# Performance work log

Measured on AMD Instinct MI355X. Metric: run time of the kernel, lower is better.

The kernel has to match this reference:

```python
import jax, jax.numpy as jnp
import numpy as np

B, S, H = 4, 8192, 576
I = 512   # moe_intermediate_size
E = 8     # num routed experts
TOP_K = 2

def setup_inputs() -> dict:
    key = jax.random.key(0)
    ks = jax.random.split(key, 8)
    sc = lambda fan_in: 1.0 / np.sqrt(fan_in)
    return {
        'x': jax.random.normal(ks[0], (B, S, H), dtype=jnp.float32),
        'shared_gate_w': jax.random.normal(ks[1], (H, I), dtype=jnp.float32) * sc(H),
        'shared_up_w':   jax.random.normal(ks[2], (H, I), dtype=jnp.float32) * sc(H),
        'shared_down_w': jax.random.normal(ks[3], (I, H), dtype=jnp.float32) * sc(I),
        'routed_gate_w': jax.random.normal(ks[4], (E, H, I), dtype=jnp.float32) * sc(H),
        'routed_up_w':   jax.random.normal(ks[5], (E, H, I), dtype=jnp.float32) * sc(H),
        'routed_down_w': jax.random.normal(ks[6], (E, I, H), dtype=jnp.float32) * sc(I),
        'router_w':      jax.random.normal(ks[7], (H, E), dtype=jnp.float32) * sc(H),
        'router_bias':   jnp.zeros((E,), dtype=jnp.float32),
    }

def reference(x, shared_gate_w, shared_up_w, shared_down_w,
              routed_gate_w, routed_up_w, routed_down_w,
              router_w, router_bias):
    b, s, h = x.shape
    flat = x.reshape(-1, h)                               # [T, H]
    T = flat.shape[0]

    # shared expert (SwiGLU)
    shared = (jax.nn.silu(flat @ shared_gate_w) * (flat @ shared_up_w)) @ shared_down_w

    # router: softmax over experts, top-k, renormalize, scatter back to dense weights
    router_logits = flat @ router_w + router_bias          # [T, E]
    routing_weights = jax.nn.softmax(router_logits, axis=1)
    topk_w, topk_i = jax.lax.top_k(routing_weights, TOP_K)  # [T, k]
    topk_w = topk_w / jnp.sum(topk_w, axis=-1, keepdims=True)
    expert_weights = jnp.zeros((T, routing_weights.shape[1]), dtype=routing_weights.dtype)
    expert_weights = expert_weights.at[jnp.arange(T)[:, None], topk_i].set(topk_w)

    # dense all-expert SwiGLU (faithful to reference: every token through every expert)
    gate = jnp.einsum('th,ehi->tei', flat, routed_gate_w)   # [T, E, I]
    up   = jnp.einsum('th,ehi->tei', flat, routed_up_w)
    expert_out = jnp.einsum('tei,eih->teh', jax.nn.silu(gate) * up, routed_down_w)  # [T, E, H]

    weighted = jnp.einsum('teh,te->th', expert_out, expert_weights)
    return (shared + weighted).reshape(b, s, h)
```

## Files before the change

### kernel.cpp

```cpp
#include <hip/hip_runtime.h>
#include <stdint.h>

#define T_TOK 32768
#define H_DIM 576
#define I_DIM 512
#define NEXP 8
#define WELEM 294912

#define NB_RT 512
#define NB_CW 7776
#define NB_GU_R 2112
#define NB_GU_S 1024

typedef __attribute__((ext_vector_type(8))) short short8;
typedef __attribute__((ext_vector_type(4))) float f32x4;
typedef __attribute__((ext_vector_type(4))) float f4;
typedef __attribute__((ext_vector_type(4))) unsigned short u16x4;

__device__ __forceinline__ unsigned short f2bf(float f) {
  union { float f; unsigned u; } v; v.f = f;
  unsigned r = (v.u + 0x7fffu + ((v.u >> 16) & 1u)) >> 16;
  return (unsigned short)r;
}

__device__ __forceinline__ void gl16(const void* g, void* l) {
  __builtin_amdgcn_global_load_lds(
      (const __attribute__((address_space(1))) unsigned*)g,
      (__attribute__((address_space(3))) unsigned*)l, 16, 0, 0);
}

__global__ __launch_bounds__(256) void prep_k(
    const float* __restrict__ x, unsigned short* __restrict__ xb,
    const float* __restrict__ rw, const float* __restrict__ rb,
    int* __restrict__ tki, float* __restrict__ tkw, int* __restrict__ counts,
    const float* __restrict__ sgw, const float* __restrict__ suw,
    const float* __restrict__ rgw, const float* __restrict__ ruw,
    const float* __restrict__ sdw, const float* __restrict__ rdw,
    unsigned short* __restrict__ wsg, unsigned short* __restrict__ wsu,
    unsigned short* __restrict__ wrg, unsigned short* __restrict__ wru,
    unsigned short* __restrict__ wsd, unsigned short* __restrict__ wrd) {
  __shared__ __align__(16) char smem[29312];
  int b = blockIdx.x, tid = threadIdx.x;
  if (b < NB_RT) {
    float* lrw = (float*)smem;
    float (*tile)[68] = (float(*)[68])(smem + 18432);
    float (*red)[8] = (float(*)[8])(smem + 27136);
    int* hist = (int*)(smem + 29184);
    for (int i = tid; i < 1152; i += 256)
      *(f4*)&lrw[i * 4] = *(const f4*)&rw[i * 4];
    if (tid < 16) hist[tid] = 0;
    int t0 = b * 64;
    float acc[NEXP] = {};
    for (int c = 0; c < 18; c++) {
      __syncthreads();
#pragma unroll
      for (int k = 0; k < 2; k++) {
        int f = tid + k * 256;
        int rgrp = f >> 8, fl = f & 255;
        int tl2 = fl >> 2, seg = fl & 3;
        int h = rgrp * 288 + c * 16 + seg * 4;
        size_t gi = (size_t)(t0 + tl2) * H_DIM + h;
        f4 v = *(const f4*)(x + gi);
        u16x4 o;
        o.x = f2bf(v.x); o.y = f2bf(v.y); o.z = f2bf(v.z); o.w = f2bf(v.w);
        *(u16x4*)(xb + gi) = o;
        int row = rgrp * 16 + seg * 4;
        tile[row + 0][tl2] = v.x; tile[row + 1][tl2] = v.y;
        tile[row + 2][tl2] = v.z; tile[row + 3][tl2] = v.w;
      }
      __syncthreads();
      if (tid < 128) {
        int half = tid >> 6, tl = tid & 63;
        int hbase = half * 288 + c * 16;
        int rbase = half * 16;
#pragma unroll
        for (int hh = 0; hh < 16; hh++) {
          float xv = tile[rbase + hh][tl];
          f4 w0 = *(const f4*)&lrw[(hbase + hh) * 8];
          f4 w1 = *(const f4*)&lrw[(hbase + hh) * 8 + 4];
          acc[0] += xv * w0.x; acc[1] += xv * w0.y;
          acc[2] += xv * w0.z; acc[3] += xv * w0.w;
          acc[4] += xv * w1.x; acc[5] += xv * w1.y;
          acc[6] += xv * w1.z; acc[7] += xv * w1.w;
        }
      }
    }
    if (tid >= 64 && tid < 128) {
      int tl = tid & 63;
#pragma unroll
      for (int e = 0; e < NEXP; e++) red[tl][e] = acc[e];
    }
    __syncthreads();
    if (tid < 64) {
      int t = t0 + tid;
      float l[NEXP];
#pragma unroll
      for (int e = 0; e < NEXP; e++) l[e] = acc[e] + red[tid][e] + rb[e];
      int e0 = 0;
#pragma unroll
      for (int e = 1; e < NEXP; e++) if (l[e] > l[e0]) e0 = e;
      int e1 = -1;
#pragma unroll
      for (int e = 0; e < NEXP; e++) {
        if (e == e0) continue;
        if (e1 < 0 || l[e] > l[e1]) e1 = e;
      }
      float w0 = 1.f / (1.f + __expf(l[e1] - l[e0]));
      tki[t * 2] = e0; tki[t * 2 + 1] = e1;
      tkw[t * 2] = w0; tkw[t * 2 + 1] = 1.f - w0;
      atomicAdd(&hist[e0], 1);
      atomicAdd(&hist[8 + e1], 1);
    }
    __syncthreads();
    if (tid < 16) atomicAdd(&counts[tid * 32], hist[tid]);
  } else {
    float (*tile)[33] = (float(*)[33])smem;
    int b0 = b - NB_RT;
    const float* src; unsigned short* dst;
    int C, bx, by;
    if (b0 < 5184) {
      int z = b0 / 288, r = b0 % 288;
      bx = r & 15; by = r >> 4; C = 512;
      if (z == 0)      { src = sgw;                            dst = wsg; }
      else if (z == 1) { src = suw;                            dst = wsu; }
      else if (z < 10) { src = rgw + (size_t)(z - 2) * WELEM;  dst = wrg + (size_t)(z - 2) * WELEM; }
      else             { src = ruw + (size_t)(z - 10) * WELEM; dst = wru + (size_t)(z - 10) * WELEM; }
    } else {
      int b2 = b0 - 5184;
      int z = b2 / 288, r = b2 % 288;
      bx = r % 18; by = r / 18; C = 576;
      src = (z == 0) ? sdw : rdw + (size_t)(z - 1) * WELEM;
      dst = (z == 0) ? wsd : wrd + (size_t)(z - 1) * WELEM;
    }
    int R = 1088 - C;
    int tx = tid & 31, ty = tid >> 5;
    int r0 = by * 32, c0 = bx * 32;
    for (int i = ty; i < 32; i += 8)
      tile[i][tx] = src[(size_t)(r0 + i) * C + c0 + tx];
    __syncthreads();
    for (int i = ty; i < 32; i += 8)
      dst[(size_t)(c0 + i) * R + r0 + tx] = f2bf(tile[tx][i]);
  }
}

__global__ __launch_bounds__(256) void scatter_k(
    const int* __restrict__ tki, const float* __restrict__ tkw,
    const int* __restrict__ counts, int* __restrict__ cursor ,
    int* __restrict__ etok, float* __restrict__ ew,
    int* __restrict__ offs16g, int* __restrict__ pcnt16g,
    int* __restrict__ pinfog) {
  __shared__ int soffs[16], hist[16], base[16], lcur[16];
  int tid = threadIdx.x;
  if (tid == 0) {
    int o = 0, p0 = 0;
    for (int s = 0; s < 16; s++) {
      int c = counts[s * 32];
      int pc = (c + 127) & ~127;
      soffs[s] = o;
      if (blockIdx.x == 0) { offs16g[s] = o; pcnt16g[s] = pc; }
      o += pc;
      if (s == 7) p0 = o;
    }
    if (blockIdx.x == 0) { pinfog[0] = p0; pinfog[1] = o - p0; }
  }
  if (tid < 16) { hist[tid] = 0; lcur[tid] = 0; }
  __syncthreads();
  int t = blockIdx.x * 256 + tid;
  int s0 = tki[t * 2], s1 = 8 + tki[t * 2 + 1];
  atomicAdd(&hist[s0], 1);
  atomicAdd(&hist[s1], 1);
  __syncthreads();
  if (tid < 16) base[tid] = atomicAdd(&cursor[tid * 32], hist[tid]);
  __syncthreads();
#pragma unroll
  for (int k = 0; k < 2; k++) {
    int s = (k == 0) ? s0 : s1;
    int r = atomicAdd(&lcur[s], 1);
    int slot = soffs[s] + base[s] + r;
    etok[slot] = t;
    ew[slot] = tkw[t * 2 + k];
  }
}

__global__ __launch_bounds__(512, 2) void gateup_k(
    const unsigned short* __restrict__ xb,
    const unsigned short* __restrict__ wg_s, const unsigned short* __restrict__ wu_s,
    const unsigned short* __restrict__ wg_r, const unsigned short* __restrict__ wu_r,
    unsigned short* __restrict__ h_s, unsigned short* __restrict__ h_r,
    const int* __restrict__ etok, const int* __restrict__ offs16,
    const int* __restrict__ pcnt16, const int* __restrict__ pinfo,
    int nrg, int p, int merged, int mchunk_r) {
  int bid = blockIdx.x;
  bool routed = bid < nrg;
  int mb, nb;
  if (routed) {
    int xcd = bid & 7, l = bid >> 3;
    mb = xcd * mchunk_r + (l >> 2);
    nb = l & 3;
    int nrows = merged ? pinfo[0] + pinfo[1] : pinfo[p];
    if (mb * 128 >= nrows) return;
  } else {
    int b2 = bid - nrg;
    int xcd = b2 & 7, l = b2 >> 3;
    mb = xcd * 32 + (l >> 2);
    nb = l & 3;
  }
  __shared__ unsigned short As[128 * 32];
  __shared__ unsigned short Bg[128 * 32];
  __shared__ unsigned short Bu[128 * 32];
  int t = threadIdx.x;
  int wv = t >> 6, lane = t & 63;
  int ar = t >> 2, seg = t & 3;
  int sg = seg ^ ((ar >> 1) & 3);
  int m0 = mb * 128 + ar;
  int tok0;
  const unsigned short *wgp, *wup;
  unsigned short* hp;
  if (routed) {
    int rl = (!merged && p) ? pinfo[0] : 0;
    int g = rl + m0;
    int s = 0;
#pragma unroll
    for (int i = 0; i < 15; i++) s += (g >= offs16[i] + pcnt16[i]) ? 1 : 0;
    int e = s & 7;
    tok0 = etok[g];
    if (tok0 < 0) tok0 = 0;
    wgp = wg_r + (size_t)e * WELEM;
    wup = wu_r + (size_t)e * WELEM;
    hp = h_r;
  } else {
    tok0 = m0;
    wgp = wg_s;
    wup = wu_s;
    hp = h_s;
  }
  const unsigned short* ga = xb + (size_t)tok0 * H_DIM + sg * 8;
  int n0 = nb * 128 + ar;
  const unsigned short* gg = wgp + (size_t)n0 * H_DIM + sg * 8;
  const unsigned short* gu = wup + (size_t)n0 * H_DIM + sg * 8;
  char* lA = (char*)As + wv * 1024;
  char* lG = (char*)Bg + wv * 1024;
  char* lU = (char*)Bu + wv * 1024;
  int fr = lane & 15, fq = lane >> 4;
  int wm = (wv >> 2) * 64, wn = (wv & 3) * 32;
  f32x4 accg[4][2] = {};
  f32x4 accu[4][2] = {};
  for (int k0 = 0; k0 < H_DIM; k0 += 32) {
    gl16(ga + k0, lA);
    gl16(gg + k0, lG);
    gl16(gu + k0, lU);
    __syncthreads();
    short8 a[4], g[2], u[2];
#pragma unroll
    for (int i = 0; i < 4; i++) {
      int r = wm + i * 16 + fr;
      a[i] = *(const short8*)&As[r * 32 + (fq ^ ((r >> 1) & 3)) * 8];
    }
#pragma unroll
    for (int j = 0; j < 2; j++) {
      int r = wn + j * 16 + fr;
      int sw = (fq ^ ((r >> 1) & 3)) * 8;
      g[j] = *(const short8*)&Bg[r * 32 + sw];
      u[j] = *(const short8*)&Bu[r * 32 + sw];
    }
#pragma unroll
    for (int i = 0; i < 4; i++)
#pragma unroll
      for (int j = 0; j < 2; j++) {
        accg[i][j] = __builtin_amdgcn_mfma_f32_16x16x32_bf16(a[i], g[j], accg[i][j], 0, 0, 0);
        accu[i][j] = __builtin_amdgcn_mfma_f32_16x16x32_bf16(a[i], u[j], accu[i][j], 0, 0, 0);
      }
    __syncthreads();
  }
#pragma unroll
  for (int i = 0; i < 4; i++)
#pragma unroll
    for (int j = 0; j < 2; j++)
#pragma unroll
      for (int r = 0; r < 4; r++) {
        int row = mb * 128 + wm + i * 16 + fq * 4 + r;
        int col = nb * 128 + wn + j * 16 + fr;
        float gv = accg[i][j][r], uv = accu[i][j][r];
        float hv = (gv / (1.f + __expf(-gv))) * uv;
        hp[(size_t)row * I_DIM + col] = f2bf(hv);
      }
}

template <int MODE>
__global__ __launch_bounds__(512, 2) void down_k(
    const unsigned short* __restrict__ hbuf, const unsigned short* __restrict__ wd,
    float* __restrict__ out, const int* __restrict__ etok, const float* __restrict__ ew,
    const int* __restrict__ offs16, const int* __restrict__ pcnt16,
    const int* __restrict__ pinfo, int p, int merged, int mchunk) {
  int bid = blockIdx.x;
  int xcd = bid & 7, l = bid >> 3;
  int mb = xcd * mchunk + l / 3;
  int nb = l % 3;
  int nrows = (MODE == 0) ? T_TOK : pinfo[p];
  if (mb * 128 >= nrows) return;
  int row_lo = (MODE == 1 && p == 1) ? pinfo[0] : 0;
  int hrow_lo = (MODE == 1 && merged) ? row_lo : 0;
  __shared__ char lds[24576];
  unsigned short* Ab = (unsigned short*)lds;
  unsigned short* Bb = (unsigned short*)(lds + 8192);
  int t = threadIdx.x;
  int wv = t >> 6, lane = t & 63;
  int ar = t >> 2, seg = t & 3;
  int sg = seg ^ ((ar >> 1) & 3);
  int e = 0;
  if (MODE == 1) {
    int g = row_lo + mb * 128 + ar;
    int s = 0;
#pragma unroll
    for (int i = 0; i < 15; i++) s += (g >= offs16[i] + pcnt16[i]) ? 1 : 0;
    e = s & 7;
  }
  const unsigned short* ga = hbuf + (size_t)(hrow_lo + mb * 128 + ar) * I_DIM + sg * 8;
  int n00 = nb * 192 + ar;
  const unsigned short* gb0 = wd + (size_t)e * WELEM + (size_t)n00 * I_DIM + sg * 8;
  const unsigned short* gb1 = gb0 + (size_t)128 * I_DIM;
  int wb = wv * 1024;
  int fr = lane & 15, fq = lane >> 4;
  int wm = (wv >> 2) * 64, wn = (wv & 3) * 48;
  f32x4 acc[4][3] = {};
  for (int k0 = 0; k0 < I_DIM; k0 += 32) {
    gl16(ga + k0, (char*)Ab + wb);
    gl16(gb0 + k0, (char*)Bb + wb);
    if (t < 256) gl16(gb1 + k0, (char*)Bb + 8192 + wb);
    __syncthreads();
    short8 a[4], b2[3];
#pragma unroll
    for (int i = 0; i < 4; i++) {
      int r = wm + i * 16 + fr;
      a[i] = *(const short8*)&Ab[r * 32 + (fq ^ ((r >> 1) & 3)) * 8];
    }
#pragma unroll
    for (int j = 0; j < 3; j++) {
      int r = wn + j * 16 + fr;
      b2[j] = *(const short8*)&Bb[r * 32 + (fq ^ ((r >> 1) & 3)) * 8];
    }
#pragma unroll
    for (int i = 0; i < 4; i++)
#pragma unroll
      for (int j = 0; j < 3; j++)
        acc[i][j] = __builtin_amdgcn_mfma_f32_16x16x32_bf16(a[i], b2[j], acc[i][j], 0, 0, 0);
    __syncthreads();
  }
  float* st = (float*)lds;
#pragma unroll
  for (int c = 0; c < 4; c++) {
    __syncthreads();
    if ((wm == 64) == (c >= 2)) {
#pragma unroll
      for (int ii = 0; ii < 2; ii++) {
        int i = (c & 1) * 2 + ii;
#pragma unroll
        for (int j = 0; j < 3; j++)
#pragma unroll
          for (int r = 0; r < 4; r++)
            st[(ii * 16 + fq * 4 + r) * 192 + wn + j * 16 + fr] = acc[i][j][r];
      }
    }
    __syncthreads();
#pragma unroll
    for (int i2 = 0; i2 < 3; i2++) {
      int s = t + i2 * 512;
      int lr = s / 48, qq = s % 48;
      int mloc = mb * 128 + c * 32 + lr;
      int colv = nb * 192 + qq * 4;
      f4 v = *(f4*)&st[lr * 192 + qq * 4];
      if (MODE == 0) {
        *(f4*)&out[(size_t)mloc * H_DIM + colv] = v;
      } else {
        int g = row_lo + mloc;
        int tok = etok[g];
        if (tok >= 0) {
          float w = ew[g];
          float* op = &out[(size_t)tok * H_DIM + colv];
          f4 o = *(f4*)op;
          o.x += w * v.x; o.y += w * v.y; o.z += w * v.z; o.w += w * v.w;
          *(f4*)op = o;
        }
      }
    }
  }
}


extern "C" void kernel_launch(void* const* d_in, const int* in_sizes, int n_in,
                              void* d_out, int out_size, void* d_ws, size_t ws_size,
                              hipStream_t stream) {
  const float* x = (const float*)d_in[0];
  const float* sgw = (const float*)d_in[1];
  const float* suw = (const float*)d_in[2];
  const float* sdw = (const float*)d_in[3];
  const float* rgw = (const float*)d_in[4];
  const float* ruw = (const float*)d_in[5];
  const float* rdw = (const float*)d_in[6];
  const float* rw = (const float*)d_in[7];
  const float* rb = (const float*)d_in[8];
  float* out = (float*)d_out;
  char* ws = (char*)d_ws;

  const size_t o_xb = 0;
  const size_t o_w = 37748736;
  const size_t w_sg = o_w;
  const size_t w_su = o_w + 589824;
  const size_t w_sd = o_w + 1179648;
  const size_t w_rg = o_w + 1769472;
  const size_t w_ru = o_w + 6488064;
  const size_t w_rd = o_w + 11206656;
  const size_t o_tki = o_w + 15925248;
  const size_t o_tkw = o_tki + 262144;
  const size_t o_meta = o_tkw + 262144;
  const size_t o_etok = o_meta + 8192;
  const size_t o_ew = o_etok + 270336;
  const size_t o_h = o_ew + 270336;
  const size_t o_hS = o_h + (size_t)67584 * 1024;
  const size_t need_t2 = o_hS;
  const size_t need_t3 = o_hS + (size_t)32768 * 1024;

  unsigned short* xb = (unsigned short*)(ws + o_xb);
  int* tki = (int*)(ws + o_tki);
  float* tkw = (float*)(ws + o_tkw);
  int* counts = (int*)(ws + o_meta);
  int* cursor = counts + 512;
  int* offs16 = counts + 1024;
  int* pcnt16 = counts + 1040;
  int* pinfo = counts + 1056;
  int* etok = (int*)(ws + o_etok);
  float* ew = (float*)(ws + o_ew);
  unsigned short* h = (unsigned short*)(ws + o_h);
  unsigned short* hS = (unsigned short*)(ws + o_hS);

  unsigned short* wsg = (unsigned short*)(ws + w_sg);
  unsigned short* wsu = (unsigned short*)(ws + w_su);
  unsigned short* wsd = (unsigned short*)(ws + w_sd);
  unsigned short* wrg = (unsigned short*)(ws + w_rg);
  unsigned short* wru = (unsigned short*)(ws + w_ru);
  unsigned short* wrd = (unsigned short*)(ws + w_rd);

  hipMemsetAsync(ws + o_meta, 0, 8192, stream);
  hipMemsetAsync(etok, 0xFF, 270336, stream);

  prep_k<<<NB_RT + NB_CW, 256, 0, stream>>>(
      x, xb, rw, rb, tki, tkw, counts,
      sgw, suw, rgw, ruw, sdw, rdw, wsg, wsu, wrg, wru, wsd, wrd);
  scatter_k<<<128, 256, 0, stream>>>(tki, tkw, counts, cursor, etok, ew,
                                     offs16, pcnt16, pinfo);

  if (ws_size >= need_t3) {
    gateup_k<<<NB_GU_R + NB_GU_S, 512, 0, stream>>>(
        xb, wsg, wsu, wrg, wru, hS, h, etok, offs16, pcnt16, pinfo,
        NB_GU_R, 0, 1, 66);
    down_k<0><<<768, 512, 0, stream>>>(hS, wsd, out, nullptr, nullptr, nullptr,
                                       nullptr, nullptr, 0, 0, 32);
    down_k<1><<<792, 512, 0, stream>>>(h, wrd, out, etok, ew, offs16,
                                       pcnt16, pinfo, 0, 1, 33);
    down_k<1><<<792, 512, 0, stream>>>(h, wrd, out, etok, ew, offs16,
                                       pcnt16, pinfo, 1, 1, 33);
  } else if (ws_size >= need_t2) {
    gateup_k<<<NB_GU_S, 512, 0, stream>>>(
        xb, wsg, wsu, wrg, wru, h, h, etok, offs16, pcnt16, pinfo,
        0, 0, 1, 66);
    down_k<0><<<768, 512, 0, stream>>>(h, wsd, out, nullptr, nullptr, nullptr,
                                       nullptr, nullptr, 0, 0, 32);
    gateup_k<<<NB_GU_R, 512, 0, stream>>>(
        xb, wsg, wsu, wrg, wru, h, h, etok, offs16, pcnt16, pinfo,
        NB_GU_R, 0, 1, 66);
    down_k<1><<<792, 512, 0, stream>>>(h, wrd, out, etok, ew, offs16,
                                       pcnt16, pinfo, 0, 1, 33);
    down_k<1><<<792, 512, 0, stream>>>(h, wrd, out, etok, ew, offs16,
                                       pcnt16, pinfo, 1, 1, 33);
  } else {
    gateup_k<<<NB_GU_S, 512, 0, stream>>>(
        xb, wsg, wsu, wrg, wru, h, h, etok, offs16, pcnt16, pinfo,
        0, 0, 0, 33);
    down_k<0><<<768, 512, 0, stream>>>(h, wsd, out, nullptr, nullptr, nullptr,
                                       nullptr, nullptr, 0, 0, 32);
    for (int p = 0; p < 2; p++) {
      gateup_k<<<1056, 512, 0, stream>>>(
          xb, wsg, wsu, wrg, wru, h, h, etok, offs16, pcnt16, pinfo,
          1056, p, 0, 33);
      down_k<1><<<792, 512, 0, stream>>>(h, wrd, out, etok, ew, offs16,
                                         pcnt16, pinfo, p, 0, 33);
    }
  }
}
```

Baseline: 336.1 us.

## Fold routing weight into gate-up output and fuse shared down into first routed pass

The routing weight is now multiplied into the SwiGLU activation in the gate-up epilogue, so the down projection no longer scales its output. A new down_k mode runs the shared-expert down GEMM (on the token's shared activation row) and the first routed down GEMM into one accumulator and writes the result directly instead of read-modify-write. This removes the separate shared down launch and one pass over the output. The cost is an extra memset of ew and a doubled K loop per tile. It relies on each token appearing exactly once in the first partition for the shared contribution to be covered.

```diff
diff --git a/kernel.cpp b/kernel.cpp
--- a/kernel.cpp
+++ b/kernel.cpp
@@ -187,8 +187,9 @@
     const unsigned short* __restrict__ wg_s, const unsigned short* __restrict__ wu_s,
     const unsigned short* __restrict__ wg_r, const unsigned short* __restrict__ wu_r,
     unsigned short* __restrict__ h_s, unsigned short* __restrict__ h_r,
-    const int* __restrict__ etok, const int* __restrict__ offs16,
-    const int* __restrict__ pcnt16, const int* __restrict__ pinfo,
+    const int* __restrict__ etok, const float* __restrict__ ew,
+    const int* __restrict__ offs16, const int* __restrict__ pcnt16,
+    const int* __restrict__ pinfo,
     int nrg, int p, int merged, int mchunk_r) {
   int bid = blockIdx.x;
   bool routed = bid < nrg;
@@ -216,6 +217,7 @@
   int tok0;
   const unsigned short *wgp, *wup;
   unsigned short* hp;
+  const float* ewp = nullptr;
   if (routed) {
     int rl = (!merged && p) ? pinfo[0] : 0;
     int g = rl + m0;
@@ -228,6 +230,7 @@
     wgp = wg_r + (size_t)e * WELEM;
     wup = wu_r + (size_t)e * WELEM;
     hp = h_r;
+    ewp = ew + rl;
   } else {
     tok0 = m0;
     wgp = wg_s;
@@ -282,14 +285,38 @@
         int col = nb * 128 + wn + j * 16 + fr;
         float gv = accg[i][j][r], uv = accu[i][j][r];
         float hv = (gv / (1.f + __expf(-gv))) * uv;
+        if (ewp) hv *= ewp[row];
         hp[(size_t)row * I_DIM + col] = f2bf(hv);
       }
 }
+
+#define DK_KLOOP(GA, GB0, GB1)                                              \
+  for (int k0 = 0; k0 < I_DIM; k0 += 32) {                                  \
+    gl16((GA) + k0, (char*)Ab + wb);                                        \
+    gl16((GB0) + k0, (char*)Bb + wb);                                       \
+    if (t < 256) gl16((GB1) + k0, (char*)Bb + 8192 + wb);                   \
+    __syncthreads();                                                        \
+    short8 a[4], b2[3];                                                     \
+    _Pragma("unroll") for (int i = 0; i < 4; i++) {                         \
+      int r = wm + i * 16 + fr;                                             \
+      a[i] = *(const short8*)&Ab[r * 32 + (fq ^ ((r >> 1) & 3)) * 8];       \
+    }                                                                       \
+    _Pragma("unroll") for (int j = 0; j < 3; j++) {                         \
+      int r = wn + j * 16 + fr;                                             \
+      b2[j] = *(const short8*)&Bb[r * 32 + (fq ^ ((r >> 1) & 3)) * 8];      \
+    }                                                                       \
+    _Pragma("unroll") for (int i = 0; i < 4; i++)                           \
+      _Pragma("unroll") for (int j = 0; j < 3; j++)                         \
+        acc[i][j] = __builtin_amdgcn_mfma_f32_16x16x32_bf16(a[i], b2[j],    \
+                                                            acc[i][j], 0, 0, 0); \
+    __syncthreads();                                                        \
+  }
 
 template <int MODE>
 __global__ __launch_bounds__(512, 2) void down_k(
-    const unsigned short* __restrict__ hbuf, const unsigned short* __restrict__ wd,
-    float* __restrict__ out, const int* __restrict__ etok, const float* __restrict__ ew,
+    const unsigned short* __restrict__ hbuf, const unsigned short* __restrict__ hS,
+    const unsigned short* __restrict__ wd, const unsigned short* __restrict__ wsd,
+    float* __restrict__ out, const int* __restrict__ etok,
     const int* __restrict__ offs16, const int* __restrict__ pcnt16,
     const int* __restrict__ pinfo, int p, int merged, int mchunk) {
   int bid = blockIdx.x;
@@ -307,45 +334,33 @@
   int wv = t >> 6, lane = t & 63;
   int ar = t >> 2, seg = t & 3;
   int sg = seg ^ ((ar >> 1) & 3);
-  int e = 0;
-  if (MODE == 1) {
+  int e = 0, tokA = 0;
+  if (MODE >= 1) {
     int g = row_lo + mb * 128 + ar;
     int s = 0;
 #pragma unroll
     for (int i = 0; i < 15; i++) s += (g >= offs16[i] + pcnt16[i]) ? 1 : 0;
     e = s & 7;
-  }
-  const unsigned short* ga = hbuf + (size_t)(hrow_lo + mb * 128 + ar) * I_DIM + sg * 8;
+    if (MODE == 2) {
+      int tk = etok[g];
+      tokA = (tk < 0) ? 0 : tk;
+    }
+  }
+  const unsigned short* gaR = hbuf + (size_t)(hrow_lo + mb * 128 + ar) * I_DIM + sg * 8;
   int n00 = nb * 192 + ar;
-  const unsigned short* gb0 = wd + (size_t)e * WELEM + (size_t)n00 * I_DIM + sg * 8;
-  const unsigned short* gb1 = gb0 + (size_t)128 * I_DIM;
+  const unsigned short* gbR = wd + (size_t)e * WELEM + (size_t)n00 * I_DIM + sg * 8;
+  const unsigned short* gbR1 = gbR + (size_t)128 * I_DIM;
   int wb = wv * 1024;
   int fr = lane & 15, fq = lane >> 4;
   int wm = (wv >> 2) * 64, wn = (wv & 3) * 48;
   f32x4 acc[4][3] = {};
-  for (int k0 = 0; k0 < I_DIM; k0 += 32) {
-    gl16(ga + k0, (char*)Ab + wb);
-    gl16(gb0 + k0, (char*)Bb + wb);
-    if (t < 256) gl16(gb1 + k0, (char*)Bb + 8192 + wb);
-    __syncthreads();
-    short8 a[4], b2[3];
-#pragma unroll
-    for (int i = 0; i < 4; i++) {
-      int r = wm + i * 16 + fr;
-      a[i] = *(const short8*)&Ab[r * 32 + (fq ^ ((r >> 1) & 3)) * 8];
-    }
-#pragma unroll
-    for (int j = 0; j < 3; j++) {
-      int r = wn + j * 16 + fr;
-      b2[j] = *(const short8*)&Bb[r * 32 + (fq ^ ((r >> 1) & 3)) * 8];
-    }
-#pragma unroll
-    for (int i = 0; i < 4; i++)
-#pragma unroll
-      for (int j = 0; j < 3; j++)
-        acc[i][j] = __builtin_amdgcn_mfma_f32_16x16x32_bf16(a[i], b2[j], acc[i][j], 0, 0, 0);
-    __syncthreads();
-  }
+  if (MODE == 2) {
+    const unsigned short* ga1 = hS + (size_t)tokA * I_DIM + sg * 8;
+    const unsigned short* gb1 = wsd + (size_t)n00 * I_DIM + sg * 8;
+    const unsigned short* gb11 = gb1 + (size_t)128 * I_DIM;
+    DK_KLOOP(ga1, gb1, gb11);
+  }
+  DK_KLOOP(gaR, gbR, gbR1);
   float* st = (float*)lds;
 #pragma unroll
   for (int c = 0; c < 4; c++) {
@@ -375,11 +390,14 @@
         int g = row_lo + mloc;
         int tok = etok[g];
         if (tok >= 0) {
-          float w = ew[g];
           float* op = &out[(size_t)tok * H_DIM + colv];
-          f4 o = *(f4*)op;
-          o.x += w * v.x; o.y += w * v.y; o.z += w * v.z; o.w += w * v.w;
-          *(f4*)op = o;
+          if (MODE == 2) {
+            *(f4*)op = v;
+          } else {
+            f4 o = *(f4*)op;
+            o.x += v.x; o.y += v.y; o.z += v.z; o.w += v.w;
+            *(f4*)op = o;
+          }
         }
       }
     }
@@ -442,6 +460,7 @@
 
   hipMemsetAsync(ws + o_meta, 0, 8192, stream);
   hipMemsetAsync(etok, 0xFF, 270336, stream);
+  hipMemsetAsync(ew, 0, 270336, stream);
 
   prep_k<<<NB_RT + NB_CW, 256, 0, stream>>>(
       x, xb, rw, rb, tki, tkw, counts,
@@ -451,39 +470,37 @@
 
   if (ws_size >= need_t3) {
     gateup_k<<<NB_GU_R + NB_GU_S, 512, 0, stream>>>(
-        xb, wsg, wsu, wrg, wru, hS, h, etok, offs16, pcnt16, pinfo,
+        xb, wsg, wsu, wrg, wru, hS, h, etok, ew, offs16, pcnt16, pinfo,
         NB_GU_R, 0, 1, 66);
-    down_k<0><<<768, 512, 0, stream>>>(hS, wsd, out, nullptr, nullptr, nullptr,
-                                       nullptr, nullptr, 0, 0, 32);
-    down_k<1><<<792, 512, 0, stream>>>(h, wrd, out, etok, ew, offs16,
-                                       pcnt16, pinfo, 0, 1, 33);
-    down_k<1><<<792, 512, 0, stream>>>(h, wrd, out, etok, ew, offs16,
-                                       pcnt16, pinfo, 1, 1, 33);
+    down_k<2><<<792, 512, 0, stream>>>(h, hS, wrd, wsd, out, etok,
+                                       offs16, pcnt16, pinfo, 0, 1, 33);
+    down_k<1><<<792, 512, 0, stream>>>(h, nullptr, wrd, nullptr, out, etok,
+                                       offs16, pcnt16, pinfo, 1, 1, 33);
   } else if (ws_size >= need_t2) {
     gateup_k<<<NB_GU_S, 512, 0, stream>>>(
-        xb, wsg, wsu, wrg, wru, h, h, etok, offs16, pcnt16, pinfo,
+        xb, wsg, wsu, wrg, wru, h, h, etok, ew, offs16, pcnt16, pinfo,
         0, 0, 1, 66);
-    down_k<0><<<768, 512, 0, stream>>>(h, wsd, out, nullptr, nullptr, nullptr,
-                                       nullptr, nullptr, 0, 0, 32);
+    down_k<0><<<768, 512, 0, stream>>>(h, nullptr, wsd, nullptr, out, etok,
+                                       offs16, pcnt16, pinfo, 0, 0, 32);
     gateup_k<<<NB_GU_R, 512, 0, stream>>>(
-        xb, wsg, wsu, wrg, wru, h, h, etok, offs16, pcnt16, pinfo,
+        xb, wsg, wsu, wrg, wru, h, h, etok, ew, offs16, pcnt16, pinfo,
         NB_GU_R, 0, 1, 66);
-    down_k<1><<<792, 512, 0, stream>>>(h, wrd, out, etok, ew, offs16,
-                                       pcnt16, pinfo, 0, 1, 33);
-    down_k<1><<<792, 512, 0, stream>>>(h, wrd, out, etok, ew, offs16,
-                                       pcnt16, pinfo, 1, 1, 33);
+    down_k<1><<<792, 512, 0, stream>>>(h, nullptr, wrd, nullptr, out, etok,
+                                       offs16, pcnt16, pinfo, 0, 1, 33);
+    down_k<1><<<792, 512, 0, stream>>>(h, nullptr, wrd, nullptr, out, etok,
+                                       offs16, pcnt16, pinfo, 1, 1, 33);
   } else {
     gateup_k<<<NB_GU_S, 512, 0, stream>>>(
-        xb, wsg, wsu, wrg, wru, h, h, etok, offs16, pcnt16, pinfo,
+        xb, wsg, wsu, wrg, wru, h, h, etok, ew, offs16, pcnt16, pinfo,
         0, 0, 0, 33);
-    down_k<0><<<768, 512, 0, stream>>>(h, wsd, out, nullptr, nullptr, nullptr,
-                                       nullptr, nullptr, 0, 0, 32);
+    down_k<0><<<768, 512, 0, stream>>>(h, nullptr, wsd, nullptr, out, etok,
+                                       offs16, pcnt16, pinfo, 0, 0, 32);
     for (int p = 0; p < 2; p++) {
       gateup_k<<<1056, 512, 0, stream>>>(
-          xb, wsg, wsu, wrg, wru, h, h, etok, offs16, pcnt16, pinfo,
+          xb, wsg, wsu, wrg, wru, h, h, etok, ew, offs16, pcnt16, pinfo,
           1056, p, 0, 33);
-      down_k<1><<<792, 512, 0, stream>>>(h, wrd, out, etok, ew, offs16,
-                                         pcnt16, pinfo, p, 0, 33);
-    }
-  }
-}
+      down_k<1><<<792, 512, 0, stream>>>(h, nullptr, wrd, nullptr, out, etok,
+                                         offs16, pcnt16, pinfo, p, 0, 33);
+    }
+  }
+}
```

Measured after the change: 327.1 us. -2.7%, faster.
